# Optimization experiments

Measured on AMD Instinct MI355X. Metric: run time of the kernel, lower is better.

Reference implementation:

```python
import jax, jax.numpy as jnp
import numpy as np

FILTER_LEN = 32
EXPECTED_SI_POWER_DB = -15
SCALE = float(np.sqrt(10.0 ** (EXPECTED_SI_POWER_DB / 10.0)))  # outputScaleFactor


def _fir(x, k):
    # x: [B,H,W,1], k: [1,FILTER_LEN,1,1]; valid conv along W (matches Conv2D kernel_size=(1,L))
    return jax.lax.conv_general_dilated(
        x, k, window_strides=(1, 1), padding='VALID',
        dimension_numbers=('NHWC', 'HWIO', 'NHWC'))


def setup_inputs() -> dict:
    key = jax.random.key(0)
    ks = jax.random.split(key, 6)
    B, H, W = 16, 64, 16384
    x_real = jax.random.normal(ks[0], (B, H, W, 1), dtype=jnp.float32)
    x_imag = jax.random.normal(ks[1], (B, H, W, 1), dtype=jnp.float32)
    # learned params (Conv2D kernels, HWIO layout, no bias)
    w_nl1 = jax.random.normal(ks[2], (1, 1, 1, 8), dtype=jnp.float32) * 0.5   # layerNL1
    w_nl2 = jax.random.normal(ks[3], (1, 1, 8, 1), dtype=jnp.float32) * 0.5   # layerNL3
    w_lin_real = jax.random.normal(ks[4], (1, FILTER_LEN, 1, 1), dtype=jnp.float32) * 0.1  # layerLIN1
    w_lin_imag = jax.random.normal(ks[5], (1, FILTER_LEN, 1, 1), dtype=jnp.float32) * 0.1  # layerLIN2
    return {'x_real': x_real, 'x_imag': x_imag, 'w_nl1': w_nl1, 'w_nl2': w_nl2,
            'w_lin_real': w_lin_real, 'w_lin_imag': w_lin_imag}


def reference(x_real, x_imag, w_nl1, w_nl2, w_lin_real, w_lin_imag):
    # complex envelope
    x_mag = jnp.sqrt(x_real * x_real + x_imag * x_imag)          # tf.math.abs
    x_phase = jnp.arctan2(x_imag, x_real)                        # tf.math.angle
    # 1x1 conv MLP on magnitude: 1 -> 8 (tanh) -> 1
    h = jnp.tanh(jnp.einsum('bhwc,co->bhwo', x_mag, w_nl1[0, 0]))
    h = jnp.einsum('bhwc,co->bhwo', h, w_nl2[0, 0])
    # re-attach phase
    xr = h * jnp.cos(x_phase)
    xi = h * jnp.sin(x_phase)
    # complex FIR: (lin_real + j*lin_imag) applied to (xr + j*xi)
    yr = _fir(xr, w_lin_real) - _fir(xi, w_lin_imag)
    yi = _fir(xi, w_lin_real) + _fir(xr, w_lin_imag)
    # stack real/imag in last dim (stands in for tf.complex), apply output scale
    return SCALE * jnp.stack([yr, yi], axis=-1)  # [B,H,W-31,1,2]
```

## Files before the change

kernel.cpp:

```cpp
#include <hip/hip_runtime.h>
#include <math.h>

#define W_IN     16384
#define FLT      32
#define W_OUT    (W_IN - FLT + 1)
#define TILE_OUT 2048
#define TILE_IN  (TILE_OUT + 64)
#define NT       256
#define N_TILES  8
#define LUT_N    2048
#define LUT_MAXM 16.0f
#define LUT_SCL  (LUT_N / LUT_MAXM)
#define OUT_SCALE 0.17782794100389228f

#define ARR_B (TILE_IN * 2)

typedef short  short8 __attribute__((ext_vector_type(8)));
typedef float  f32x4  __attribute__((ext_vector_type(4)));

__device__ __forceinline__ int swz16(int b) {
    return b ^ (((b >> 7) & 7) << 4);
}

__device__ __forceinline__ void bsplit(float x, unsigned short& h, unsigned short& l) {
    const unsigned u = __float_as_uint(x);
    h = (unsigned short)(u >> 16);
    const float rem = x - __uint_as_float(u & 0xffff0000u);
    l = (unsigned short)(__float_as_uint(rem) >> 16);
}

__global__ void build_lut_kernel(const float* __restrict__ w1,
                                 const float* __restrict__ w2,
                                 float* __restrict__ lut) {
    const int k = blockIdx.x * blockDim.x + threadIdx.x;
    if (k >= LUT_N) return;
    float c1[8], c2[8];
#pragma unroll
    for (int j = 0; j < 8; ++j) { c1[j] = w1[j]; c2[j] = w2[j]; }
    if (k == 0) {
        float g0 = 0.f;
#pragma unroll
        for (int j = 0; j < 8; ++j) g0 += c2[j] * c1[j];
        lut[0] = g0;
    } else {
        const float m = (float)k * (LUT_MAXM / LUT_N);
        float h = 0.f;
#pragma unroll
        for (int j = 0; j < 8; ++j) h += c2[j] * tanhf(c1[j] * m);
        lut[k] = h / m;
    }
}

#define MFMA(a, b, c) __builtin_amdgcn_mfma_f32_16x16x32_bf16((a), (b), (c), 0, 0, 0)

__global__ __launch_bounds__(NT, 4)
void fused_env_mlp_fir_kernel(const float* __restrict__ xr,
                              const float* __restrict__ xi,
                              const float* __restrict__ lut_g,
                              const float* __restrict__ wlr,
                              const float* __restrict__ wli,
                              float* __restrict__ out)
{
    __shared__ __align__(16) unsigned short sx[4 * TILE_IN];
    __shared__ float slut[LUT_N];
    __shared__ float staps[64];

    const int bid    = blockIdx.x;
    const int row    = bid >> 3;
    const int tile   = bid & 7;
    const int tstart = tile * TILE_OUT;
    const int tid    = threadIdx.x;
    const int lane   = tid & 63;

    for (int i = tid; i < LUT_N / 4; i += NT)
        *(float4*)(slut + 4 * i) = *(const float4*)(lut_g + 4 * i);
    if (tid < 32)       staps[tid] = wlr[tid] * OUT_SCALE;
    else if (tid < 64)  staps[tid] = wli[tid - 32] * OUT_SCALE;
    __syncthreads();

    const float* __restrict__ xr_row = xr + (size_t)row * W_IN;
    const float* __restrict__ xi_row = xi + (size_t)row * W_IN;

    for (int c = tid; c < TILE_IN / 4; c += NT) {
        const int g = tstart + 4 * c;
        float4 vr, vi;
        if (g + 3 < W_IN) {
            vr = *(const float4*)(xr_row + g);
            vi = *(const float4*)(xi_row + g);
        } else {
            vr = make_float4(0.f, 0.f, 0.f, 0.f);
            vi = make_float4(0.f, 0.f, 0.f, 0.f);
        }
        const float ar[4] = {vr.x, vr.y, vr.z, vr.w};
        const float ai[4] = {vi.x, vi.y, vi.z, vi.w};
        unsigned short rha[4], rla[4], iha[4], ila[4];
#pragma unroll
        for (int e = 0; e < 4; ++e) {
            const float a = ar[e], b = ai[e];
            const float s = fmaxf(fmaf(a, a, b * b), 1e-30f);
            const float rs = rsqrtf(s);
            const float mag  = s * rs;
            const float idxf = mag * LUT_SCL;
            int i = (int)idxf;
            i = min(i, LUT_N - 2);
            const float fr = idxf - (float)i;
            const float g0 = slut[i], g1 = slut[i + 1];
            const float gg = fmaf(fr, g1 - g0, g0);
            bsplit(a * gg, rha[e], rla[e]);
            bsplit(b * gg, iha[e], ila[e]);
        }
        const int pb = swz16(8 * c);
        char* sb = (char*)sx;
        *(ushort4*)(sb + 0 * ARR_B + pb) = make_ushort4(rha[0], rha[1], rha[2], rha[3]);
        *(ushort4*)(sb + 1 * ARR_B + pb) = make_ushort4(rla[0], rla[1], rla[2], rla[3]);
        *(ushort4*)(sb + 2 * ARR_B + pb) = make_ushort4(iha[0], iha[1], iha[2], iha[3]);
        *(ushort4*)(sb + 3 * ARR_B + pb) = make_ushort4(ila[0], ila[1], ila[2], ila[3]);
    }

    short8 frh[2], frl[2], fih[2], fil[2];
    {
        const int fm  = lane & 15;
        const int fk0 = (lane >> 4) << 3;
#pragma unroll
        for (int c = 0; c < 2; ++c) {
#pragma unroll
            for (int e = 0; e < 8; ++e) {
                const int t = fk0 + e - fm + 32 * c;
                const bool v = ((unsigned)t < 32u);
                const int ti = v ? t : 0;
                const float fr_ = v ? staps[ti]      : 0.f;
                const float fi_ = v ? staps[32 + ti] : 0.f;
                unsigned short h, l;
                bsplit(fr_, h, l); frh[c][e] = (short)h; frl[c][e] = (short)l;
                bsplit(fi_, h, l); fih[c][e] = (short)h; fil[c][e] = (short)l;
            }
        }
    }
    __syncthreads();

    const int wid = tid >> 6;
    const int rr  = lane & 15;
    const int jj  = lane >> 4;
    float* __restrict__ out_row = out + (size_t)row * (W_OUT * 2);
    const int remain = W_OUT - tstart;
    const char* sb = (const char*)sx;

    const short8 sgn = {(short)0x8000, (short)0x8000, (short)0x8000, (short)0x8000,
                        (short)0x8000, (short)0x8000, (short)0x8000, (short)0x8000};

#pragma unroll
    for (int gi = 0; gi < 2; ++gi) {
        const int grp = wid + 4 * gi;
        const int s   = grp << 8;
        const int bl = 2 * s + 32 * rr + 16 * jj;
        const int a0 = swz16(bl);
        const int a1 = swz16(bl + 64);
        const short8 xrh0 = *(const short8*)(sb + 0 * ARR_B + a0);
        const short8 xrh1 = *(const short8*)(sb + 0 * ARR_B + a1);
        const short8 xrl0 = *(const short8*)(sb + 1 * ARR_B + a0);
        const short8 xrl1 = *(const short8*)(sb + 1 * ARR_B + a1);
        const short8 xih0 = *(const short8*)(sb + 2 * ARR_B + a0);
        const short8 xih1 = *(const short8*)(sb + 2 * ARR_B + a1);
        const short8 xil0 = *(const short8*)(sb + 3 * ARR_B + a0);
        const short8 xil1 = *(const short8*)(sb + 3 * ARR_B + a1);
        const short8 nih0 = xih0 ^ sgn;
        const short8 nih1 = xih1 ^ sgn;
        const short8 nil0 = xil0 ^ sgn;
        const short8 nil1 = xil1 ^ sgn;

        f32x4 accr = {0.f, 0.f, 0.f, 0.f};
        f32x4 acci = {0.f, 0.f, 0.f, 0.f};
        accr = MFMA(frh[0], xrh0, accr);  acci = MFMA(frh[0], xih0, acci);
        accr = MFMA(frh[1], xrh1, accr);  acci = MFMA(frh[1], xih1, acci);
        accr = MFMA(fih[0], nih0, accr);  acci = MFMA(fih[0], xrh0, acci);
        accr = MFMA(fih[1], nih1, accr);  acci = MFMA(fih[1], xrh1, acci);
        accr = MFMA(frh[0], xrl0, accr);  acci = MFMA(frh[0], xil0, acci);
        accr = MFMA(frh[1], xrl1, accr);  acci = MFMA(frh[1], xil1, acci);
        accr = MFMA(frl[0], xrh0, accr);  acci = MFMA(frl[0], xih0, acci);
        accr = MFMA(frl[1], xrh1, accr);  acci = MFMA(frl[1], xih1, acci);
        accr = MFMA(fih[0], nil0, accr);  acci = MFMA(fih[0], xrl0, acci);
        accr = MFMA(fih[1], nil1, accr);  acci = MFMA(fih[1], xrl1, acci);
        accr = MFMA(fil[0], nih0, accr);  acci = MFMA(fil[0], xrh0, acci);
        accr = MFMA(fil[1], nih1, accr);  acci = MFMA(fil[1], xrh1, acci);

        const int p0 = s + 16 * rr + 4 * jj;
        float* dst = out_row + (size_t)(tstart + p0) * 2;
        if (p0 + 3 < remain) {
            *(float4*)(dst)     = make_float4(accr[0], acci[0], accr[1], acci[1]);
            *(float4*)(dst + 4) = make_float4(accr[2], acci[2], accr[3], acci[3]);
        } else {
#pragma unroll
            for (int q = 0; q < 4; ++q)
                if (p0 + q < remain)
                    *(float2*)(dst + 2 * q) = make_float2(accr[q], acci[q]);
        }
    }
}

extern "C" void kernel_launch(void* const* d_in, const int* in_sizes, int n_in,
                              void* d_out, int out_size, void* d_ws, size_t ws_size,
                              hipStream_t stream) {
    const float* xr  = (const float*)d_in[0];
    const float* xi  = (const float*)d_in[1];
    const float* w1  = (const float*)d_in[2];
    const float* w2  = (const float*)d_in[3];
    const float* wlr = (const float*)d_in[4];
    const float* wli = (const float*)d_in[5];
    float* out = (float*)d_out;
    float* lut = (float*)d_ws;

    build_lut_kernel<<<dim3(LUT_N / NT), dim3(NT), 0, stream>>>(w1, w2, lut);

    const int rows = 16 * 64;
    fused_env_mlp_fir_kernel<<<dim3(rows * N_TILES), dim3(NT), 0, stream>>>(
        xr, xi, lut, wlr, wli, out);
}
```

Baseline: 253.4 us.

## Process four tiles per block with register prefetch of next tile

Each block now handles four consecutive row-tiles instead of one. The LUT and taps are loaded once per block, and the global loads for the next tile are issued into registers before the current tile's MFMA phase so memory latency overlaps compute. This amortises the per-block setup (LUT copy, filter fragment build) and hides load latency. In exchange the grid is four times smaller, register pressure rises from the prefetch buffers, and there are two barriers per tile.

```diff
diff --git a/kernel.cpp b/kernel.cpp
--- a/kernel.cpp
+++ b/kernel.cpp
@@ -8,6 +8,7 @@
 #define TILE_IN  (TILE_OUT + 64)
 #define NT       256
 #define N_TILES  8
+#define UPB      4
 #define LUT_N    2048
 #define LUT_MAXM 16.0f
 #define LUT_SCL  (LUT_N / LUT_MAXM)
@@ -52,6 +53,27 @@
 }
 
 #define MFMA(a, b, c) __builtin_amdgcn_mfma_f32_16x16x32_bf16((a), (b), (c), 0, 0, 0)
+
+#define LOAD_UNIT(u) do {                                                   \
+    const int _row = (u) >> 3, _tile = (u) & 7;                             \
+    const int _ts  = _tile * TILE_OUT;                                      \
+    const float* __restrict__ _xr = xr + (size_t)_row * W_IN;               \
+    const float* __restrict__ _xi = xi + (size_t)_row * W_IN;               \
+    _Pragma("unroll")                                                       \
+    for (int _it = 0; _it < 3; ++_it) {                                     \
+        const int _c = tid + NT * _it;                                      \
+        float4 _zr = make_float4(0.f, 0.f, 0.f, 0.f);                       \
+        float4 _zi = make_float4(0.f, 0.f, 0.f, 0.f);                       \
+        if (_c < TILE_IN / 4) {                                             \
+            const int _g = _ts + 4 * _c;                                    \
+            if (_g + 3 < W_IN) {                                            \
+                _zr = *(const float4*)(_xr + _g);                           \
+                _zi = *(const float4*)(_xi + _g);                           \
+            }                                                               \
+        }                                                                   \
+        pvr[_it] = _zr; pvi[_it] = _zi;                                     \
+    }                                                                       \
+} while (0)
 
 __global__ __launch_bounds__(NT, 4)
 void fused_env_mlp_fir_kernel(const float* __restrict__ xr,
@@ -65,57 +87,18 @@
     __shared__ float slut[LUT_N];
     __shared__ float staps[64];
 
-    const int bid    = blockIdx.x;
-    const int row    = bid >> 3;
-    const int tile   = bid & 7;
-    const int tstart = tile * TILE_OUT;
-    const int tid    = threadIdx.x;
-    const int lane   = tid & 63;
+    const int tid  = threadIdx.x;
+    const int lane = tid & 63;
+    const int unit0 = blockIdx.x * UPB;
+
+    float4 pvr[3], pvi[3];
+    LOAD_UNIT(unit0);
 
     for (int i = tid; i < LUT_N / 4; i += NT)
         *(float4*)(slut + 4 * i) = *(const float4*)(lut_g + 4 * i);
     if (tid < 32)       staps[tid] = wlr[tid] * OUT_SCALE;
     else if (tid < 64)  staps[tid] = wli[tid - 32] * OUT_SCALE;
     __syncthreads();
-
-    const float* __restrict__ xr_row = xr + (size_t)row * W_IN;
-    const float* __restrict__ xi_row = xi + (size_t)row * W_IN;
-
-    for (int c = tid; c < TILE_IN / 4; c += NT) {
-        const int g = tstart + 4 * c;
-        float4 vr, vi;
-        if (g + 3 < W_IN) {
-            vr = *(const float4*)(xr_row + g);
-            vi = *(const float4*)(xi_row + g);
-        } else {
-            vr = make_float4(0.f, 0.f, 0.f, 0.f);
-            vi = make_float4(0.f, 0.f, 0.f, 0.f);
-        }
-        const float ar[4] = {vr.x, vr.y, vr.z, vr.w};
-        const float ai[4] = {vi.x, vi.y, vi.z, vi.w};
-        unsigned short rha[4], rla[4], iha[4], ila[4];
-#pragma unroll
-        for (int e = 0; e < 4; ++e) {
-            const float a = ar[e], b = ai[e];
-            const float s = fmaxf(fmaf(a, a, b * b), 1e-30f);
-            const float rs = rsqrtf(s);
-            const float mag  = s * rs;
-            const float idxf = mag * LUT_SCL;
-            int i = (int)idxf;
-            i = min(i, LUT_N - 2);
-            const float fr = idxf - (float)i;
-            const float g0 = slut[i], g1 = slut[i + 1];
-            const float gg = fmaf(fr, g1 - g0, g0);
-            bsplit(a * gg, rha[e], rla[e]);
-            bsplit(b * gg, iha[e], ila[e]);
-        }
-        const int pb = swz16(8 * c);
-        char* sb = (char*)sx;
-        *(ushort4*)(sb + 0 * ARR_B + pb) = make_ushort4(rha[0], rha[1], rha[2], rha[3]);
-        *(ushort4*)(sb + 1 * ARR_B + pb) = make_ushort4(rla[0], rla[1], rla[2], rla[3]);
-        *(ushort4*)(sb + 2 * ARR_B + pb) = make_ushort4(iha[0], iha[1], iha[2], iha[3]);
-        *(ushort4*)(sb + 3 * ARR_B + pb) = make_ushort4(ila[0], ila[1], ila[2], ila[3]);
-    }
 
     short8 frh[2], frl[2], fih[2], fil[2];
     {
@@ -136,64 +119,109 @@
             }
         }
     }
-    __syncthreads();
 
     const int wid = tid >> 6;
     const int rr  = lane & 15;
     const int jj  = lane >> 4;
-    float* __restrict__ out_row = out + (size_t)row * (W_OUT * 2);
-    const int remain = W_OUT - tstart;
-    const char* sb = (const char*)sx;
-
+    const char* sbr = (const char*)sx;
     const short8 sgn = {(short)0x8000, (short)0x8000, (short)0x8000, (short)0x8000,
                         (short)0x8000, (short)0x8000, (short)0x8000, (short)0x8000};
 
-#pragma unroll
-    for (int gi = 0; gi < 2; ++gi) {
-        const int grp = wid + 4 * gi;
-        const int s   = grp << 8;
-        const int bl = 2 * s + 32 * rr + 16 * jj;
-        const int a0 = swz16(bl);
-        const int a1 = swz16(bl + 64);
-        const short8 xrh0 = *(const short8*)(sb + 0 * ARR_B + a0);
-        const short8 xrh1 = *(const short8*)(sb + 0 * ARR_B + a1);
-        const short8 xrl0 = *(const short8*)(sb + 1 * ARR_B + a0);
-        const short8 xrl1 = *(const short8*)(sb + 1 * ARR_B + a1);
-        const short8 xih0 = *(const short8*)(sb + 2 * ARR_B + a0);
-        const short8 xih1 = *(const short8*)(sb + 2 * ARR_B + a1);
-        const short8 xil0 = *(const short8*)(sb + 3 * ARR_B + a0);
-        const short8 xil1 = *(const short8*)(sb + 3 * ARR_B + a1);
-        const short8 nih0 = xih0 ^ sgn;
-        const short8 nih1 = xih1 ^ sgn;
-        const short8 nil0 = xil0 ^ sgn;
-        const short8 nil1 = xil1 ^ sgn;
-
-        f32x4 accr = {0.f, 0.f, 0.f, 0.f};
-        f32x4 acci = {0.f, 0.f, 0.f, 0.f};
-        accr = MFMA(frh[0], xrh0, accr);  acci = MFMA(frh[0], xih0, acci);
-        accr = MFMA(frh[1], xrh1, accr);  acci = MFMA(frh[1], xih1, acci);
-        accr = MFMA(fih[0], nih0, accr);  acci = MFMA(fih[0], xrh0, acci);
-        accr = MFMA(fih[1], nih1, accr);  acci = MFMA(fih[1], xrh1, acci);
-        accr = MFMA(frh[0], xrl0, accr);  acci = MFMA(frh[0], xil0, acci);
-        accr = MFMA(frh[1], xrl1, accr);  acci = MFMA(frh[1], xil1, acci);
-        accr = MFMA(frl[0], xrh0, accr);  acci = MFMA(frl[0], xih0, acci);
-        accr = MFMA(frl[1], xrh1, accr);  acci = MFMA(frl[1], xih1, acci);
-        accr = MFMA(fih[0], nil0, accr);  acci = MFMA(fih[0], xrl0, acci);
-        accr = MFMA(fih[1], nil1, accr);  acci = MFMA(fih[1], xrl1, acci);
-        accr = MFMA(fil[0], nih0, accr);  acci = MFMA(fil[0], xrh0, acci);
-        accr = MFMA(fil[1], nih1, accr);  acci = MFMA(fil[1], xrh1, acci);
-
-        const int p0 = s + 16 * rr + 4 * jj;
-        float* dst = out_row + (size_t)(tstart + p0) * 2;
-        if (p0 + 3 < remain) {
-            *(float4*)(dst)     = make_float4(accr[0], acci[0], accr[1], acci[1]);
-            *(float4*)(dst + 4) = make_float4(accr[2], acci[2], accr[3], acci[3]);
-        } else {
-#pragma unroll
-            for (int q = 0; q < 4; ++q)
-                if (p0 + q < remain)
-                    *(float2*)(dst + 2 * q) = make_float2(accr[q], acci[q]);
+    for (int t = 0; t < UPB; ++t) {
+        const int unit   = unit0 + t;
+        const int row    = unit >> 3;
+        const int tstart = (unit & 7) * TILE_OUT;
+
+#pragma unroll
+        for (int it = 0; it < 3; ++it) {
+            const int c = tid + NT * it;
+            if (c < TILE_IN / 4) {
+                const float4 vr = pvr[it], vi = pvi[it];
+                const float ar[4] = {vr.x, vr.y, vr.z, vr.w};
+                const float ai[4] = {vi.x, vi.y, vi.z, vi.w};
+                unsigned short rha[4], rla[4], iha[4], ila[4];
+#pragma unroll
+                for (int e = 0; e < 4; ++e) {
+                    const float a = ar[e], b = ai[e];
+                    const float s = fmaxf(fmaf(a, a, b * b), 1e-30f);
+                    const float rs = rsqrtf(s);
+                    const float mag  = s * rs;
+                    const float idxf = mag * LUT_SCL;
+                    int i = (int)idxf;
+                    i = min(i, LUT_N - 2);
+                    const float fr = idxf - (float)i;
+                    const float g0 = slut[i], g1 = slut[i + 1];
+                    const float gg = fmaf(fr, g1 - g0, g0);
+                    bsplit(a * gg, rha[e], rla[e]);
+                    bsplit(b * gg, iha[e], ila[e]);
+                }
+                const int pb = swz16(8 * c);
+                char* sb = (char*)sx;
+                *(ushort4*)(sb + 0 * ARR_B + pb) = make_ushort4(rha[0], rha[1], rha[2], rha[3]);
+                *(ushort4*)(sb + 1 * ARR_B + pb) = make_ushort4(rla[0], rla[1], rla[2], rla[3]);
+                *(ushort4*)(sb + 2 * ARR_B + pb) = make_ushort4(iha[0], iha[1], iha[2], iha[3]);
+                *(ushort4*)(sb + 3 * ARR_B + pb) = make_ushort4(ila[0], ila[1], ila[2], ila[3]);
+            }
         }
+
+        if (t != UPB - 1) LOAD_UNIT(unit + 1);
+
+        asm volatile("s_waitcnt lgkmcnt(0)" ::: "memory");
+        __builtin_amdgcn_s_barrier();
+
+        float* __restrict__ out_row = out + (size_t)row * (W_OUT * 2);
+        const int remain = W_OUT - tstart;
+
+#pragma unroll
+        for (int gi = 0; gi < 2; ++gi) {
+            const int grp = wid + 4 * gi;
+            const int s   = grp << 8;
+            const int bl = 2 * s + 32 * rr + 16 * jj;
+            const int a0 = swz16(bl);
+            const int a1 = swz16(bl + 64);
+            const short8 xrh0 = *(const short8*)(sbr + 0 * ARR_B + a0);
+            const short8 xrh1 = *(const short8*)(sbr + 0 * ARR_B + a1);
+            const short8 xrl0 = *(const short8*)(sbr + 1 * ARR_B + a0);
+            const short8 xrl1 = *(const short8*)(sbr + 1 * ARR_B + a1);
+            const short8 xih0 = *(const short8*)(sbr + 2 * ARR_B + a0);
+            const short8 xih1 = *(const short8*)(sbr + 2 * ARR_B + a1);
+            const short8 xil0 = *(const short8*)(sbr + 3 * ARR_B + a0);
+            const short8 xil1 = *(const short8*)(sbr + 3 * ARR_B + a1);
+            const short8 nih0 = xih0 ^ sgn;
+            const short8 nih1 = xih1 ^ sgn;
+            const short8 nil0 = xil0 ^ sgn;
+            const short8 nil1 = xil1 ^ sgn;
+
+            f32x4 accr = {0.f, 0.f, 0.f, 0.f};
+            f32x4 acci = {0.f, 0.f, 0.f, 0.f};
+            accr = MFMA(frh[0], xrh0, accr);  acci = MFMA(frh[0], xih0, acci);
+            accr = MFMA(frh[1], xrh1, accr);  acci = MFMA(frh[1], xih1, acci);
+            accr = MFMA(fih[0], nih0, accr);  acci = MFMA(fih[0], xrh0, acci);
+            accr = MFMA(fih[1], nih1, accr);  acci = MFMA(fih[1], xrh1, acci);
+            accr = MFMA(frh[0], xrl0, accr);  acci = MFMA(frh[0], xil0, acci);
+            accr = MFMA(frh[1], xrl1, accr);  acci = MFMA(frh[1], xil1, acci);
+            accr = MFMA(frl[0], xrh0, accr);  acci = MFMA(frl[0], xih0, acci);
+            accr = MFMA(frl[1], xrh1, accr);  acci = MFMA(frl[1], xih1, acci);
+            accr = MFMA(fih[0], nil0, accr);  acci = MFMA(fih[0], xrl0, acci);
+            accr = MFMA(fih[1], nil1, accr);  acci = MFMA(fih[1], xrl1, acci);
+            accr = MFMA(fil[0], nih0, accr);  acci = MFMA(fil[0], xrh0, acci);
+            accr = MFMA(fil[1], nih1, accr);  acci = MFMA(fil[1], xrh1, acci);
+
+            const int p0 = s + 16 * rr + 4 * jj;
+            float* dst = out_row + (size_t)(tstart + p0) * 2;
+            if (p0 + 3 < remain) {
+                *(float4*)(dst)     = make_float4(accr[0], acci[0], accr[1], acci[1]);
+                *(float4*)(dst + 4) = make_float4(accr[2], acci[2], accr[3], acci[3]);
+            } else {
+#pragma unroll
+                for (int q = 0; q < 4; ++q)
+                    if (p0 + q < remain)
+                        *(float2*)(dst + 2 * q) = make_float2(accr[q], acci[q]);
+            }
+        }
+
+        asm volatile("s_waitcnt lgkmcnt(0)" ::: "memory");
+        __builtin_amdgcn_s_barrier();
     }
 }
 
@@ -212,6 +240,7 @@
     build_lut_kernel<<<dim3(LUT_N / NT), dim3(NT), 0, stream>>>(w1, w2, lut);
 
     const int rows = 16 * 64;
-    fused_env_mlp_fir_kernel<<<dim3(rows * N_TILES), dim3(NT), 0, stream>>>(
+    const int blocks = rows * N_TILES / UPB;
+    fused_env_mlp_fir_kernel<<<dim3(blocks), dim3(NT), 0, stream>>>(
         xr, xi, lut, wlr, wli, out);
 }
```

Result: no change. 250.7 us (-1.1%).

## Load inputs directly into MFMA fragments, drop LDS staging, prefetch next group

Applied to the files above, without the earlier changes.

Each lane now loads its own B-fragment x values from global memory, computes the envelope and bf16 hi/lo split in registers, and feeds the MFMAs directly, with no LDS tile or extra barrier. The next group's inputs are prefetched while the current group computes. Halo elements are loaded twice by neighbouring lanes. The LUT stores (value, delta) pairs so interpolation needs one LDS read. A separate accumulator for the subtracted term replaces the sign-flip XORs. The cost is redundant envelope computation on the overlapped halo and more registers per thread.

```diff
diff --git a/kernel.cpp b/kernel.cpp
--- a/kernel.cpp
+++ b/kernel.cpp
@@ -4,23 +4,18 @@
 #define W_IN     16384
 #define FLT      32
 #define W_OUT    (W_IN - FLT + 1)
-#define TILE_OUT 2048
-#define TILE_IN  (TILE_OUT + 64)
 #define NT       256
-#define N_TILES  8
+#define GRP      256
+#define GPW      4
+#define NGRP     64
 #define LUT_N    2048
 #define LUT_MAXM 16.0f
 #define LUT_SCL  (LUT_N / LUT_MAXM)
 #define OUT_SCALE 0.17782794100389228f
-
-#define ARR_B (TILE_IN * 2)
+#define PMAX     (W_IN - 8)
 
 typedef short  short8 __attribute__((ext_vector_type(8)));
 typedef float  f32x4  __attribute__((ext_vector_type(4)));
-
-__device__ __forceinline__ int swz16(int b) {
-    return b ^ (((b >> 7) & 7) << 4);
-}
 
 __device__ __forceinline__ void bsplit(float x, unsigned short& h, unsigned short& l) {
     const unsigned u = __float_as_uint(x);
@@ -29,107 +24,87 @@
     l = (unsigned short)(__float_as_uint(rem) >> 16);
 }
 
+__device__ __forceinline__ float gfun(const float* c1, const float* c2, int k) {
+    if (k == 0) {
+        float g0 = 0.f;
+#pragma unroll
+        for (int j = 0; j < 8; ++j) g0 += c2[j] * c1[j];
+        return g0;
+    }
+    const float m = (float)k * (LUT_MAXM / LUT_N);
+    float h = 0.f;
+#pragma unroll
+    for (int j = 0; j < 8; ++j) h += c2[j] * tanhf(c1[j] * m);
+    return h / m;
+}
+
 __global__ void build_lut_kernel(const float* __restrict__ w1,
                                  const float* __restrict__ w2,
-                                 float* __restrict__ lut) {
+                                 float2* __restrict__ lut2) {
     const int k = blockIdx.x * blockDim.x + threadIdx.x;
     if (k >= LUT_N) return;
     float c1[8], c2[8];
 #pragma unroll
     for (int j = 0; j < 8; ++j) { c1[j] = w1[j]; c2[j] = w2[j]; }
-    if (k == 0) {
-        float g0 = 0.f;
-#pragma unroll
-        for (int j = 0; j < 8; ++j) g0 += c2[j] * c1[j];
-        lut[0] = g0;
-    } else {
-        const float m = (float)k * (LUT_MAXM / LUT_N);
-        float h = 0.f;
-#pragma unroll
-        for (int j = 0; j < 8; ++j) h += c2[j] * tanhf(c1[j] * m);
-        lut[k] = h / m;
-    }
+    const float g0 = gfun(c1, c2, k);
+    const float g1 = gfun(c1, c2, k + 1);
+    lut2[k] = make_float2(g0, g1 - g0);
 }
 
 #define MFMA(a, b, c) __builtin_amdgcn_mfma_f32_16x16x32_bf16((a), (b), (c), 0, 0, 0)
+
+__device__ __forceinline__ void env8(const float2* __restrict__ slut,
+                                     float4 r0, float4 r1, float4 i0, float4 i1,
+                                     short8& xh, short8& xl, short8& yh, short8& yl) {
+    const float ar[8] = {r0.x, r0.y, r0.z, r0.w, r1.x, r1.y, r1.z, r1.w};
+    const float ai[8] = {i0.x, i0.y, i0.z, i0.w, i1.x, i1.y, i1.z, i1.w};
+#pragma unroll
+    for (int e = 0; e < 8; ++e) {
+        const float a = ar[e], b = ai[e];
+        const float s = fmaxf(fmaf(a, a, b * b), 1e-30f);
+        const float rs = rsqrtf(s);
+        const float mag  = s * rs;
+        const float idxf = mag * LUT_SCL;
+        int i = (int)idxf;
+        i = min(i, LUT_N - 1);
+        const float fr = idxf - (float)i;
+        const float2 gd = slut[i];
+        const float gg = fmaf(fr, gd.y, gd.x);
+        unsigned short h, l;
+        bsplit(a * gg, h, l); xh[e] = (short)h; xl[e] = (short)l;
+        bsplit(b * gg, h, l); yh[e] = (short)h; yl[e] = (short)l;
+    }
+}
 
 __global__ __launch_bounds__(NT, 4)
 void fused_env_mlp_fir_kernel(const float* __restrict__ xr,
                               const float* __restrict__ xi,
-                              const float* __restrict__ lut_g,
+                              const float2* __restrict__ lut2,
                               const float* __restrict__ wlr,
                               const float* __restrict__ wli,
                               float* __restrict__ out)
 {
-    __shared__ __align__(16) unsigned short sx[4 * TILE_IN];
-    __shared__ float slut[LUT_N];
-    __shared__ float staps[64];
-
-    const int bid    = blockIdx.x;
-    const int row    = bid >> 3;
-    const int tile   = bid & 7;
-    const int tstart = tile * TILE_OUT;
-    const int tid    = threadIdx.x;
-    const int lane   = tid & 63;
-
-    for (int i = tid; i < LUT_N / 4; i += NT)
-        *(float4*)(slut + 4 * i) = *(const float4*)(lut_g + 4 * i);
-    if (tid < 32)       staps[tid] = wlr[tid] * OUT_SCALE;
-    else if (tid < 64)  staps[tid] = wli[tid - 32] * OUT_SCALE;
-    __syncthreads();
-
-    const float* __restrict__ xr_row = xr + (size_t)row * W_IN;
-    const float* __restrict__ xi_row = xi + (size_t)row * W_IN;
-
-    for (int c = tid; c < TILE_IN / 4; c += NT) {
-        const int g = tstart + 4 * c;
-        float4 vr, vi;
-        if (g + 3 < W_IN) {
-            vr = *(const float4*)(xr_row + g);
-            vi = *(const float4*)(xi_row + g);
-        } else {
-            vr = make_float4(0.f, 0.f, 0.f, 0.f);
-            vi = make_float4(0.f, 0.f, 0.f, 0.f);
-        }
-        const float ar[4] = {vr.x, vr.y, vr.z, vr.w};
-        const float ai[4] = {vi.x, vi.y, vi.z, vi.w};
-        unsigned short rha[4], rla[4], iha[4], ila[4];
-#pragma unroll
-        for (int e = 0; e < 4; ++e) {
-            const float a = ar[e], b = ai[e];
-            const float s = fmaxf(fmaf(a, a, b * b), 1e-30f);
-            const float rs = rsqrtf(s);
-            const float mag  = s * rs;
-            const float idxf = mag * LUT_SCL;
-            int i = (int)idxf;
-            i = min(i, LUT_N - 2);
-            const float fr = idxf - (float)i;
-            const float g0 = slut[i], g1 = slut[i + 1];
-            const float gg = fmaf(fr, g1 - g0, g0);
-            bsplit(a * gg, rha[e], rla[e]);
-            bsplit(b * gg, iha[e], ila[e]);
-        }
-        const int pb = swz16(8 * c);
-        char* sb = (char*)sx;
-        *(ushort4*)(sb + 0 * ARR_B + pb) = make_ushort4(rha[0], rha[1], rha[2], rha[3]);
-        *(ushort4*)(sb + 1 * ARR_B + pb) = make_ushort4(rla[0], rla[1], rla[2], rla[3]);
-        *(ushort4*)(sb + 2 * ARR_B + pb) = make_ushort4(iha[0], iha[1], iha[2], iha[3]);
-        *(ushort4*)(sb + 3 * ARR_B + pb) = make_ushort4(ila[0], ila[1], ila[2], ila[3]);
-    }
+    __shared__ float2 slut[LUT_N];
+
+    const int tid  = threadIdx.x;
+    const int lane = tid & 63;
+    const int rr   = lane & 15;
+    const int jj   = lane >> 4;
+
+    for (int i = tid; i < LUT_N / 2; i += NT)
+        ((float4*)slut)[i] = ((const float4*)lut2)[i];
 
     short8 frh[2], frl[2], fih[2], fil[2];
     {
-        const int fm  = lane & 15;
-        const int fk0 = (lane >> 4) << 3;
 #pragma unroll
         for (int c = 0; c < 2; ++c) {
 #pragma unroll
             for (int e = 0; e < 8; ++e) {
-                const int t = fk0 + e - fm + 32 * c;
+                const int t = 8 * jj + e - rr + 32 * c;
                 const bool v = ((unsigned)t < 32u);
                 const int ti = v ? t : 0;
-                const float fr_ = v ? staps[ti]      : 0.f;
-                const float fi_ = v ? staps[32 + ti] : 0.f;
+                const float fr_ = v ? wlr[ti] * OUT_SCALE : 0.f;
+                const float fi_ = v ? wli[ti] * OUT_SCALE : 0.f;
                 unsigned short h, l;
                 bsplit(fr_, h, l); frh[c][e] = (short)h; frl[c][e] = (short)l;
                 bsplit(fi_, h, l); fih[c][e] = (short)h; fil[c][e] = (short)l;
@@ -138,61 +113,72 @@
     }
     __syncthreads();
 
-    const int wid = tid >> 6;
-    const int rr  = lane & 15;
-    const int jj  = lane >> 4;
+    const int row = blockIdx.x >> 2;
+    const int g0  = ((blockIdx.x & 3) * 4 + (tid >> 6)) * GPW;
+    const float* __restrict__ xr_row = xr + (size_t)row * W_IN;
+    const float* __restrict__ xi_row = xi + (size_t)row * W_IN;
     float* __restrict__ out_row = out + (size_t)row * (W_OUT * 2);
-    const int remain = W_OUT - tstart;
-    const char* sb = (const char*)sx;
-
-    const short8 sgn = {(short)0x8000, (short)0x8000, (short)0x8000, (short)0x8000,
-                        (short)0x8000, (short)0x8000, (short)0x8000, (short)0x8000};
-
-#pragma unroll
-    for (int gi = 0; gi < 2; ++gi) {
-        const int grp = wid + 4 * gi;
-        const int s   = grp << 8;
-        const int bl = 2 * s + 32 * rr + 16 * jj;
-        const int a0 = swz16(bl);
-        const int a1 = swz16(bl + 64);
-        const short8 xrh0 = *(const short8*)(sb + 0 * ARR_B + a0);
-        const short8 xrh1 = *(const short8*)(sb + 0 * ARR_B + a1);
-        const short8 xrl0 = *(const short8*)(sb + 1 * ARR_B + a0);
-        const short8 xrl1 = *(const short8*)(sb + 1 * ARR_B + a1);
-        const short8 xih0 = *(const short8*)(sb + 2 * ARR_B + a0);
-        const short8 xih1 = *(const short8*)(sb + 2 * ARR_B + a1);
-        const short8 xil0 = *(const short8*)(sb + 3 * ARR_B + a0);
-        const short8 xil1 = *(const short8*)(sb + 3 * ARR_B + a1);
-        const short8 nih0 = xih0 ^ sgn;
-        const short8 nih1 = xih1 ^ sgn;
-        const short8 nil0 = xil0 ^ sgn;
-        const short8 nil1 = xil1 ^ sgn;
-
-        f32x4 accr = {0.f, 0.f, 0.f, 0.f};
-        f32x4 acci = {0.f, 0.f, 0.f, 0.f};
-        accr = MFMA(frh[0], xrh0, accr);  acci = MFMA(frh[0], xih0, acci);
-        accr = MFMA(frh[1], xrh1, accr);  acci = MFMA(frh[1], xih1, acci);
-        accr = MFMA(fih[0], nih0, accr);  acci = MFMA(fih[0], xrh0, acci);
-        accr = MFMA(fih[1], nih1, accr);  acci = MFMA(fih[1], xrh1, acci);
-        accr = MFMA(frh[0], xrl0, accr);  acci = MFMA(frh[0], xil0, acci);
-        accr = MFMA(frh[1], xrl1, accr);  acci = MFMA(frh[1], xil1, acci);
-        accr = MFMA(frl[0], xrh0, accr);  acci = MFMA(frl[0], xih0, acci);
-        accr = MFMA(frl[1], xrh1, accr);  acci = MFMA(frl[1], xih1, acci);
-        accr = MFMA(fih[0], nil0, accr);  acci = MFMA(fih[0], xrl0, acci);
-        accr = MFMA(fih[1], nil1, accr);  acci = MFMA(fih[1], xrl1, acci);
-        accr = MFMA(fil[0], nih0, accr);  acci = MFMA(fil[0], xrh0, acci);
-        accr = MFMA(fil[1], nih1, accr);  acci = MFMA(fil[1], xrh1, acci);
+
+    const int lofs = 8 * (2 * rr + jj);
+    int pA = g0 * GRP + lofs;
+
+    float4 pv0, pv1, pv2, pv3, pv4, pv5, pv6, pv7;
+    {
+        const int a = min(pA, PMAX);
+        const int b = min(pA + 32, PMAX);
+        pv0 = *(const float4*)(xr_row + a);     pv1 = *(const float4*)(xr_row + a + 4);
+        pv2 = *(const float4*)(xr_row + b);     pv3 = *(const float4*)(xr_row + b + 4);
+        pv4 = *(const float4*)(xi_row + a);     pv5 = *(const float4*)(xi_row + a + 4);
+        pv6 = *(const float4*)(xi_row + b);     pv7 = *(const float4*)(xi_row + b + 4);
+    }
+
+#pragma unroll
+    for (int gi = 0; gi < GPW; ++gi) {
+        const int s = (g0 + gi) * GRP;
+
+        short8 xrh0, xrl0, xih0, xil0, xrh1, xrl1, xih1, xil1;
+        env8(slut, pv0, pv1, pv4, pv5, xrh0, xrl0, xih0, xil0);
+        env8(slut, pv2, pv3, pv6, pv7, xrh1, xrl1, xih1, xil1);
+
+        if (gi != GPW - 1) {
+            const int pA2 = pA + GRP;
+            const int a = min(pA2, PMAX);
+            const int b = min(pA2 + 32, PMAX);
+            pv0 = *(const float4*)(xr_row + a); pv1 = *(const float4*)(xr_row + a + 4);
+            pv2 = *(const float4*)(xr_row + b); pv3 = *(const float4*)(xr_row + b + 4);
+            pv4 = *(const float4*)(xi_row + a); pv5 = *(const float4*)(xi_row + a + 4);
+            pv6 = *(const float4*)(xi_row + b); pv7 = *(const float4*)(xi_row + b + 4);
+            pA = pA2;
+        }
+
+        f32x4 acr = {0.f, 0.f, 0.f, 0.f};
+        f32x4 aci = {0.f, 0.f, 0.f, 0.f};
+        f32x4 acs = {0.f, 0.f, 0.f, 0.f};
+        aci = MFMA(frh[0], xih0, aci); acr = MFMA(frh[0], xrh0, acr); acs = MFMA(fih[0], xih0, acs);
+        aci = MFMA(frh[1], xih1, aci); acr = MFMA(frh[1], xrh1, acr); acs = MFMA(fih[1], xih1, acs);
+        aci = MFMA(fih[0], xrh0, aci); acr = MFMA(frh[0], xrl0, acr); acs = MFMA(fih[0], xil0, acs);
+        aci = MFMA(fih[1], xrh1, aci); acr = MFMA(frh[1], xrl1, acr); acs = MFMA(fih[1], xil1, acs);
+        aci = MFMA(frh[0], xil0, aci); acr = MFMA(frl[0], xrh0, acr); acs = MFMA(fil[0], xih0, acs);
+        aci = MFMA(frh[1], xil1, aci); acr = MFMA(frl[1], xrh1, acr); acs = MFMA(fil[1], xih1, acs);
+        aci = MFMA(frl[0], xih0, aci);
+        aci = MFMA(frl[1], xih1, aci);
+        aci = MFMA(fil[0], xrh0, aci);
+        aci = MFMA(fil[1], xrh1, aci);
+        aci = MFMA(fih[0], xrl0, aci);
+        aci = MFMA(fih[1], xrl1, aci);
 
         const int p0 = s + 16 * rr + 4 * jj;
-        float* dst = out_row + (size_t)(tstart + p0) * 2;
-        if (p0 + 3 < remain) {
-            *(float4*)(dst)     = make_float4(accr[0], acci[0], accr[1], acci[1]);
-            *(float4*)(dst + 4) = make_float4(accr[2], acci[2], accr[3], acci[3]);
+        float* dst = out_row + (size_t)p0 * 2;
+        if (s + GRP <= W_OUT) {
+            *(float4*)(dst)     = make_float4(acr[0] - acs[0], aci[0],
+                                              acr[1] - acs[1], aci[1]);
+            *(float4*)(dst + 4) = make_float4(acr[2] - acs[2], aci[2],
+                                              acr[3] - acs[3], aci[3]);
         } else {
 #pragma unroll
             for (int q = 0; q < 4; ++q)
-                if (p0 + q < remain)
-                    *(float2*)(dst + 2 * q) = make_float2(accr[q], acci[q]);
+                if (p0 + q < W_OUT)
+                    *(float2*)(dst + 2 * q) = make_float2(acr[q] - acs[q], aci[q]);
         }
     }
 }
@@ -207,11 +193,12 @@
     const float* wlr = (const float*)d_in[4];
     const float* wli = (const float*)d_in[5];
     float* out = (float*)d_out;
-    float* lut = (float*)d_ws;
-
-    build_lut_kernel<<<dim3(LUT_N / NT), dim3(NT), 0, stream>>>(w1, w2, lut);
+    float2* lut2 = (float2*)d_ws;
+
+    build_lut_kernel<<<dim3(LUT_N / NT), dim3(NT), 0, stream>>>(w1, w2, lut2);
 
     const int rows = 16 * 64;
-    fused_env_mlp_fir_kernel<<<dim3(rows * N_TILES), dim3(NT), 0, stream>>>(
-        xr, xi, lut, wlr, wli, out);
-}
+    const int blocks = rows * (NGRP / (4 * GPW));
+    fused_env_mlp_fir_kernel<<<dim3(blocks), dim3(NT), 0, stream>>>(
+        xr, xi, lut2, wlr, wli, out);
+}
```

New measurement: 277.4 us. +9.4%, slower.
